# Optimization experiments

Measured on AMD Instinct MI355X. Metric: run time of the kernel, lower is better.

## Reference

```python
import jax, jax.numpy as jnp
import numpy as np
from jax import lax

V, D, L, H, MAXLEN = 32000, 512, 6, 8, 1024
DH = D // H
DFF = 4 * D
B, T = 8, 1024


def _ln(x, g, b, eps=1e-5):
    m = jnp.mean(x, axis=-1, keepdims=True)
    v = jnp.var(x, axis=-1, keepdims=True)
    return (x - m) * lax.rsqrt(v + eps) * g + b


def setup_inputs() -> dict:
    key = jax.random.key(0)
    ks = jax.random.split(key, 16)
    s = 0.02
    inp = {
        "idx": jax.random.randint(ks[0], (B, T), 0, V, dtype=jnp.int32),
        "wte": jax.random.normal(ks[1], (V, D), jnp.float32) * s,   # tied with head
        "wpe": jax.random.normal(ks[2], (MAXLEN, D), jnp.float32) * s,
        # per-layer stacked params [L, ...]
        "ln1_g": jnp.ones((L, D), jnp.float32),
        "ln1_b": jnp.zeros((L, D), jnp.float32),
        "w_qkv": jax.random.normal(ks[3], (L, D, 3 * D), jnp.float32) * s,
        "b_qkv": jnp.zeros((L, 3 * D), jnp.float32),
        "w_ao": jax.random.normal(ks[4], (L, D, D), jnp.float32) * s,
        "b_ao": jnp.zeros((L, D), jnp.float32),
        "ln2_g": jnp.ones((L, D), jnp.float32),
        "ln2_b": jnp.zeros((L, D), jnp.float32),
        "w_fc": jax.random.normal(ks[5], (L, D, DFF), jnp.float32) * s,
        "b_fc": jnp.zeros((L, DFF), jnp.float32),
        "w_pr": jax.random.normal(ks[6], (L, DFF, D), jnp.float32) * s,
        "b_pr": jnp.zeros((L, D), jnp.float32),
        "lnf_g": jnp.ones((D,), jnp.float32),
        "lnf_b": jnp.zeros((D,), jnp.float32),
    }
    return inp


def reference(idx, wte, wpe, ln1_g, ln1_b, w_qkv, b_qkv, w_ao, b_ao,
              ln2_g, ln2_b, w_fc, b_fc, w_pr, b_pr, lnf_g, lnf_b):
    Bx, Tx = idx.shape
    x = wte[idx] + wpe[:Tx]                      # [B,T,D]
    causal = jnp.tril(jnp.ones((Tx, Tx), bool))  # [T,T]
    scale = 1.0 / np.sqrt(DH)

    def block(x, p):
        (g1, b1, wqkv, bqkv, wao, bao, g2, b2, wfc, bfc, wpr, bpr) = p
        h = _ln(x, g1, b1)
        qkv = h @ wqkv + bqkv                    # [B,T,3D]
        q, k, v = jnp.split(qkv, 3, axis=-1)
        q = q.reshape(Bx, Tx, H, DH)
        k = k.reshape(Bx, Tx, H, DH)
        v = v.reshape(Bx, Tx, H, DH)
        att = jnp.einsum('bqhd,bkhd->bhqk', q, k) * scale
        att = jnp.where(causal, att, -jnp.inf)
        att = jax.nn.softmax(att, axis=-1)
        y = jnp.einsum('bhqk,bkhd->bqhd', att, v).reshape(Bx, Tx, D)
        x = x + y @ wao + bao
        h = _ln(x, g2, b2)
        h = jax.nn.gelu(h @ wfc + bfc, approximate=False)
        x = x + h @ wpr + bpr
        return x, None

    params = (ln1_g, ln1_b, w_qkv, b_qkv, w_ao, b_ao,
              ln2_g, ln2_b, w_fc, b_fc, w_pr, b_pr)
    x, _ = lax.scan(block, x, params)
    x = _ln(x, lnf_g, lnf_b)
    logits = x @ wte.T                           # tied head, [B,T,V]
    return logits
```

## Files before the change

### kernel.cpp

```cpp
#include <hip/hip_runtime.h>
#include <hip/hip_bf16.h>
#include <math.h>

#define V_   32000
#define D_   512
#define L_   6
#define H_   8
#define DH_  64
#define DFF_ 2048
#define B_   8
#define T_   1024
#define BT_  (B_*T_)

typedef __attribute__((ext_vector_type(4))) float f32x4;
typedef __attribute__((ext_vector_type(8))) short short8;
using bf16_t = __hip_bfloat16;

__device__ __forceinline__ float b2f(unsigned short u) {
    union { unsigned int i; float f; } v; v.i = ((unsigned int)u) << 16; return v.f;
}
__device__ __forceinline__ unsigned short f2b(float f) {
    bf16_t h = __float2bfloat16(f);
    return *reinterpret_cast<unsigned short*>(&h);
}
__device__ __forceinline__ void gl16(const void* g, void* l) {
    __builtin_amdgcn_global_load_lds((const __attribute__((address_space(1))) void*)g,
                                     (__attribute__((address_space(3))) void*)l, 16, 0, 0);
}
__device__ __forceinline__ float gelu_exact(float v) {
    return 0.5f * v * (1.0f + erff(v * 0.70710678118654752f));
}

__global__ __launch_bounds__(128) void embed_ln_kernel(
        const int* __restrict__ idx, const float* __restrict__ wte,
        const float* __restrict__ wpe, const float* __restrict__ g,
        const float* __restrict__ bb, float* __restrict__ x,
        bf16_t* __restrict__ hout) {
    int bt = blockIdx.x;
    int tt = bt & (T_ - 1);
    int tok = idx[bt];
    int i = threadIdx.x;
    float4 a = ((const float4*)(wte + (size_t)tok * D_))[i];
    float4 p = ((const float4*)(wpe + (size_t)tt * D_))[i];
    float4 v = make_float4(a.x + p.x, a.y + p.y, a.z + p.z, a.w + p.w);
    ((float4*)(x + (size_t)bt * D_))[i] = v;

    float s  = v.x + v.y + v.z + v.w;
    float sq = v.x*v.x + v.y*v.y + v.z*v.z + v.w*v.w;
    #pragma unroll
    for (int o = 32; o > 0; o >>= 1) {
        s  += __shfl_down(s,  o);
        sq += __shfl_down(sq, o);
    }
    __shared__ float ss[2], ssq[2];
    if ((i & 63) == 0) { ss[i >> 6] = s; ssq[i >> 6] = sq; }
    __syncthreads();
    float mean = (ss[0] + ss[1]) * (1.0f / D_);
    float var  = (ssq[0] + ssq[1]) * (1.0f / D_) - mean * mean;
    float rstd = rsqrtf(var + 1e-5f);
    float4 gg = ((const float4*)g)[i];
    float4 b2 = ((const float4*)bb)[i];
    ushort4 o4;
    o4.x = f2b((v.x - mean) * rstd * gg.x + b2.x);
    o4.y = f2b((v.y - mean) * rstd * gg.y + b2.y);
    o4.z = f2b((v.z - mean) * rstd * gg.z + b2.z);
    o4.w = f2b((v.w - mean) * rstd * gg.w + b2.w);
    ((ushort4*)(hout + (size_t)bt * D_))[i] = o4;
}

__global__ __launch_bounds__(256) void conv_kernel(
        const float* __restrict__ s, bf16_t* __restrict__ d, int n4) {
    int i = blockIdx.x * 256 + threadIdx.x;
    if (i >= n4) return;
    float4 f = ((const float4*)s)[i];
    ushort4 u = make_ushort4(f2b(f.x), f2b(f.y), f2b(f.z), f2b(f.w));
    ((ushort4*)d)[i] = u;
}

__global__ __launch_bounds__(256) void tconv_kernel(
        const float* __restrict__ src, bf16_t* __restrict__ dst, int K, int N) {
    size_t ls = (size_t)K * N;
    const float* s = src + blockIdx.z * ls;
    bf16_t* d = dst + blockIdx.z * ls;
    __shared__ float tile[32][33];
    int n0 = blockIdx.x * 32, k0 = blockIdx.y * 32;
    int c = threadIdx.x & 31, r8 = threadIdx.x >> 5;
    #pragma unroll
    for (int i = 0; i < 4; ++i) {
        int r = r8 + i * 8;
        tile[r][c] = s[(size_t)(k0 + r) * N + n0 + c];
    }
    __syncthreads();
    #pragma unroll
    for (int i = 0; i < 4; ++i) {
        int r = r8 + i * 8;
        d[(size_t)(n0 + r) * K + k0 + c] = __float2bfloat16(tile[c][r]);
    }
}

__global__ __launch_bounds__(256) void vtrans_kernel(
        const bf16_t* __restrict__ qkv, bf16_t* __restrict__ vt) {
    const unsigned short* q = (const unsigned short*)qkv;
    unsigned short* d = (unsigned short*)vt;
    __shared__ unsigned short tile[32][33];
    int bh = blockIdx.z;
    int b  = bh >> 3, h = bh & 7;
    int t0 = blockIdx.x * 32, d0 = blockIdx.y * 32;
    int c = threadIdx.x & 31, r8 = threadIdx.x >> 5;
    #pragma unroll
    for (int i = 0; i < 4; ++i) {
        int r = r8 + i * 8;
        tile[r][c] = q[(size_t)(b * T_ + t0 + r) * (3 * D_) + 2 * D_ + h * DH_ + d0 + c];
    }
    __syncthreads();
    #pragma unroll
    for (int i = 0; i < 4; ++i) {
        int r = r8 + i * 8;
        d[(size_t)(bh * DH_ + d0 + r) * T_ + t0 + c] = tile[c][r];
    }
}

template<int BK, int ACT, bool OBF, bool RES, bool CONVB>
__global__ __launch_bounds__(256) void mm_kernel(
        const bf16_t* __restrict__ A,
        const bf16_t* __restrict__ Bt,
        const float*  __restrict__ Bf,
        const float*  __restrict__ bias,
        const float*  __restrict__ res,
        void* __restrict__ Cout,
        int M, int N, int K)
{
    constexpr int SLOTS = BK / 8;
    constexpr int CH    = BK / 16;
    __shared__ __align__(16) unsigned short As[128 * BK];
    __shared__ __align__(16) unsigned short Bs[128 * BK];
    const int nwg = gridDim.x;
    const int orig = blockIdx.x;
    const int q8 = nwg >> 3, r8 = nwg & 7;
    const int xcd = orig & 7, lin = orig >> 3;
    const int wg = (xcd < r8) ? xcd * (q8 + 1) + lin
                              : r8 * (q8 + 1) + (xcd - r8) * q8 + lin;
    const int gym = M >> 7;
    const int by = wg % gym;
    const int bx = wg / gym;

    const int t    = threadIdx.x;
    const int row0 = by * 128;
    const int col0 = bx * 128;
    const int lane = t & 63;
    const int wid  = t >> 6;
    const int wm   = (wid & 1) * 64;
    const int wn   = (wid >> 1) * 64;
    const int fr   = lane & 15;
    const int fq   = lane >> 4;

    f32x4 acc[4][4];
    #pragma unroll
    for (int m = 0; m < 4; ++m)
        #pragma unroll
        for (int n = 0; n < 4; ++n)
            acc[m][n] = (f32x4)(0.0f);

    const unsigned short* Ab  = (const unsigned short*)A;
    const unsigned short* Btb = (const unsigned short*)Bt;

    for (int k0 = 0; k0 < K; k0 += BK) {
        __syncthreads();
        #pragma unroll
        for (int i = 0; i < CH; ++i) {
            int c = t + i * 256;
            int row = c / SLOTS;
            int sl  = (c & (SLOTS - 1)) ^ (row & 7);
            gl16(Ab + (size_t)(row0 + row) * K + k0 + sl * 8, As + (size_t)c * 8);
        }
        if (!CONVB) {
            #pragma unroll
            for (int i = 0; i < CH; ++i) {
                int c = t + i * 256;
                int row = c / SLOTS;
                int sl  = (c & (SLOTS - 1)) ^ (row & 7);
                gl16(Btb + (size_t)(col0 + row) * K + k0 + sl * 8, Bs + (size_t)c * 8);
            }
        } else {
            #pragma unroll
            for (int i = 0; i < CH; ++i) {
                int c = t + i * 256;
                int row = c / SLOTS;
                int sl  = (c & (SLOTS - 1)) ^ (row & 7);
                const float* sp = Bf + (size_t)(col0 + row) * K + k0 + sl * 8;
                float4 f0 = ((const float4*)sp)[0];
                float4 f1 = ((const float4*)sp)[1];
                short8 pk;
                pk[0] = f2b(f0.x); pk[1] = f2b(f0.y); pk[2] = f2b(f0.z); pk[3] = f2b(f0.w);
                pk[4] = f2b(f1.x); pk[5] = f2b(f1.y); pk[6] = f2b(f1.z); pk[7] = f2b(f1.w);
                *(short8*)(Bs + (size_t)c * 8) = pk;
            }
        }
        __syncthreads();

        #pragma unroll
        for (int kk = 0; kk < BK / 32; ++kk) {
            short8 av[4], bv[4];
            #pragma unroll
            for (int m = 0; m < 4; ++m) {
                int R = wm + m * 16 + fr;
                int sl = (kk * 4 + fq) ^ (fr & 7);
                av[m] = *(const short8*)(As + (size_t)R * BK + sl * 8);
            }
            #pragma unroll
            for (int n = 0; n < 4; ++n) {
                int R = wn + n * 16 + fr;
                int sl = (kk * 4 + fq) ^ (fr & 7);
                bv[n] = *(const short8*)(Bs + (size_t)R * BK + sl * 8);
            }
            #pragma unroll
            for (int m = 0; m < 4; ++m)
                #pragma unroll
                for (int n = 0; n < 4; ++n)
                    acc[m][n] = __builtin_amdgcn_mfma_f32_16x16x32_bf16(av[m], bv[n], acc[m][n], 0, 0, 0);
        }
    }

    #pragma unroll
    for (int n = 0; n < 4; ++n) {
        int col = col0 + wn + n * 16 + fr;
        float bb = bias ? bias[col] : 0.0f;
        #pragma unroll
        for (int m = 0; m < 4; ++m) {
            int rbase = row0 + wm + m * 16 + fq * 4;
            #pragma unroll
            for (int r = 0; r < 4; ++r) {
                float v = acc[m][n][r] + bb;
                if (ACT == 1) v = gelu_exact(v);
                size_t off = (size_t)(rbase + r) * N + col;
                if (RES) v += res[off];
                if (OBF) ((bf16_t*)Cout)[off] = __float2bfloat16(v);
                else     ((float*)Cout)[off]  = v;
            }
        }
    }
}

__global__ __launch_bounds__(512) void mm_ln_kernel(
        const bf16_t* __restrict__ A,
        const bf16_t* __restrict__ Bt,
        const float*  __restrict__ bias,
        float*        __restrict__ xio,
        const float*  __restrict__ g,
        const float*  __restrict__ lb,
        bf16_t*       __restrict__ hout,
        int M, int K)
{
    __shared__ __align__(16) unsigned short As[32 * 64];
    __shared__ __align__(16) unsigned short Bs[512 * 64];
    __shared__ float stats[32][8][2];

    const int row0 = blockIdx.x * 32;
    const int t    = threadIdx.x;
    const int lane = t & 63;
    const int w    = t >> 6;
    const int fr   = lane & 15;
    const int fq   = lane >> 4;

    const unsigned short* Ab  = (const unsigned short*)A;
    const unsigned short* Btb = (const unsigned short*)Bt;

    f32x4 acc[2][4];
    #pragma unroll
    for (int m = 0; m < 2; ++m)
        #pragma unroll
        for (int n = 0; n < 4; ++n)
            acc[m][n] = (f32x4)(0.0f);

    for (int k0 = 0; k0 < K; k0 += 64) {
        __syncthreads();
        if (t < 256) {
            int c = t;
            int row = c >> 3, sl = (c & 7) ^ (row & 7);
            gl16(Ab + (size_t)(row0 + row) * K + k0 + sl * 8, As + (size_t)c * 8);
        }
        #pragma unroll
        for (int i = 0; i < 8; ++i) {
            int c = t + i * 512;
            int row = c >> 3, sl = (c & 7) ^ (row & 7);
            gl16(Btb + (size_t)row * K + k0 + sl * 8, Bs + (size_t)c * 8);
        }
        __syncthreads();

        #pragma unroll
        for (int kk = 0; kk < 2; ++kk) {
            int sl = (kk * 4 + fq) ^ (fr & 7);
            short8 av[2], bv[4];
            #pragma unroll
            for (int m = 0; m < 2; ++m)
                av[m] = *(const short8*)(As + (size_t)(m * 16 + fr) * 64 + sl * 8);
            #pragma unroll
            for (int n = 0; n < 4; ++n)
                bv[n] = *(const short8*)(Bs + (size_t)(w * 64 + n * 16 + fr) * 64 + sl * 8);
            #pragma unroll
            for (int m = 0; m < 2; ++m)
                #pragma unroll
                for (int n = 0; n < 4; ++n)
                    acc[m][n] = __builtin_amdgcn_mfma_f32_16x16x32_bf16(av[m], bv[n], acc[m][n], 0, 0, 0);
        }
    }

    float vv[2][4][4];
    #pragma unroll
    for (int m = 0; m < 2; ++m) {
        #pragma unroll
        for (int r = 0; r < 4; ++r) {
            int rowl = m * 16 + fq * 4 + r;
            float ps = 0.0f, pq = 0.0f;
            #pragma unroll
            for (int n = 0; n < 4; ++n) {
                int col = w * 64 + n * 16 + fr;
                float v = acc[m][n][r] + bias[col] +
                          xio[(size_t)(row0 + rowl) * D_ + col];
                vv[m][n][r] = v;
                ps += v; pq += v * v;
            }
            ps += __shfl_xor(ps, 1); pq += __shfl_xor(pq, 1);
            ps += __shfl_xor(ps, 2); pq += __shfl_xor(pq, 2);
            ps += __shfl_xor(ps, 4); pq += __shfl_xor(pq, 4);
            ps += __shfl_xor(ps, 8); pq += __shfl_xor(pq, 8);
            if (fr == 0) { stats[rowl][w][0] = ps; stats[rowl][w][1] = pq; }
        }
    }
    __syncthreads();

    #pragma unroll
    for (int m = 0; m < 2; ++m) {
        #pragma unroll
        for (int r = 0; r < 4; ++r) {
            int rowl = m * 16 + fq * 4 + r;
            float su = 0.0f, sq = 0.0f;
            #pragma unroll
            for (int ww = 0; ww < 8; ++ww) {
                su += stats[rowl][ww][0];
                sq += stats[rowl][ww][1];
            }
            float mean = su * (1.0f / D_);
            float var  = sq * (1.0f / D_) - mean * mean;
            float rstd = rsqrtf(var + 1e-5f);
            #pragma unroll
            for (int n = 0; n < 4; ++n) {
                int col = w * 64 + n * 16 + fr;
                float v = vv[m][n][r];
                size_t off = (size_t)(row0 + rowl) * D_ + col;
                xio[off] = v;
                hout[off] = __float2bfloat16((v - mean) * rstd * g[col] + lb[col]);
            }
        }
    }
}

#define MM8_PHASE(MH, NH, HALF, SRCB, R0, DSTB)                               \
  {                                                                           \
    short8 af[2][4]; short8 bg[2][2];                                         \
    _Pragma("unroll")                                                         \
    for (int ks = 0; ks < 2; ++ks) {                                          \
      _Pragma("unroll")                                                       \
      for (int m = 0; m < 4; ++m) {                                           \
        int row = ((MH)*4 + m)*32 + wm*16 + fr;                               \
        int sl  = (ks*4 + fq) ^ (fr & 7);                                     \
        af[ks][m] = *(const short8*)(curA + (size_t)row*64 + (size_t)sl*8);   \
      }                                                                       \
      _Pragma("unroll")                                                       \
      for (int n = 0; n < 2; ++n) {                                           \
        int col = ((NH)*2 + n)*64 + wn*16 + fr;                               \
        int sl  = (ks*4 + fq) ^ (fr & 7);                                     \
        bg[ks][n] = *(const short8*)(curB + (size_t)col*64 + (size_t)sl*8);   \
      }                                                                       \
    }                                                                         \
    if (pf) {                                                                 \
      _Pragma("unroll")                                                       \
      for (int i = 0; i < 2; ++i) {                                           \
        int c = (HALF)*1024 + i*512 + t;                                      \
        int row = c >> 3, sl = (c & 7) ^ (row & 7);                           \
        gl16(SRCB + (size_t)((R0) + row)*K + k0n + sl*8,                      \
             DSTB + (size_t)c*8);                                             \
      }                                                                       \
      asm volatile("s_waitcnt vmcnt(2)" ::: "memory");                        \
    } else if ((MH) == 0 && (NH) == 0) {                                      \
      asm volatile("s_waitcnt vmcnt(0)" ::: "memory");                        \
    }                                                                         \
    asm volatile("s_barrier" ::: "memory");                                   \
    asm volatile("s_waitcnt lgkmcnt(0)" ::: "memory");                        \
    __builtin_amdgcn_sched_barrier(0);                                        \
    __builtin_amdgcn_s_setprio(1);                                            \
    _Pragma("unroll")                                                         \
    for (int ks = 0; ks < 2; ++ks)                                            \
      _Pragma("unroll")                                                       \
      for (int m = 0; m < 4; ++m)                                             \
        _Pragma("unroll")                                                     \
        for (int n = 0; n < 2; ++n)                                           \
          acc[(MH)*4+m][(NH)*2+n] = __builtin_amdgcn_mfma_f32_16x16x32_bf16(  \
              af[ks][m], bg[ks][n], acc[(MH)*4+m][(NH)*2+n], 0, 0, 0);        \
    __builtin_amdgcn_s_setprio(0);                                            \
    __builtin_amdgcn_sched_barrier(0);                                        \
    asm volatile("s_barrier" ::: "memory");                                   \
  }

template<int ACT, bool OBF>
__global__ __launch_bounds__(512) void mm8_kernel(
        const bf16_t* __restrict__ A,
        const bf16_t* __restrict__ Bt,
        const float*  __restrict__ bias,
        void* __restrict__ Cout,
        int M, int N, int K)
{
    __shared__ __align__(16) unsigned short sA[2][256 * 64];
    __shared__ __align__(16) unsigned short sB[2][256 * 64];

    const int nwg = gridDim.x;
    const int orig = blockIdx.x;
    const int q8 = nwg >> 3, r8 = nwg & 7;
    const int xcd = orig & 7, lin = orig >> 3;
    const int wg = (xcd < r8) ? xcd * (q8 + 1) + lin
                              : r8 * (q8 + 1) + (xcd - r8) * q8 + lin;
    const int gym = M >> 8;
    const int by = wg % gym;
    const int bx = wg / gym;
    const int row0 = by * 256;
    const int col0 = bx * 256;

    const int t    = threadIdx.x;
    const int lane = t & 63;
    const int wid  = t >> 6;
    const int wm   = wid >> 2;
    const int wn   = wid & 3;
    const int fr   = lane & 15;
    const int fq   = lane >> 4;

    const unsigned short* Ab = (const unsigned short*)A;
    const unsigned short* Bb = (const unsigned short*)Bt;

    f32x4 acc[8][4];
    #pragma unroll
    for (int m = 0; m < 8; ++m)
        #pragma unroll
        for (int n = 0; n < 4; ++n)
            acc[m][n] = (f32x4)(0.0f);

    const int NK = K >> 6;

    #pragma unroll
    for (int h = 0; h < 2; ++h)
        #pragma unroll
        for (int i = 0; i < 2; ++i) {
            int c = h * 1024 + i * 512 + t;
            int row = c >> 3, sl = (c & 7) ^ (row & 7);
            gl16(Ab + (size_t)(row0 + row) * K + sl * 8, &sA[0][(size_t)c * 8]);
            gl16(Bb + (size_t)(col0 + row) * K + sl * 8, &sB[0][(size_t)c * 8]);
        }
    asm volatile("s_waitcnt vmcnt(0)" ::: "memory");
    asm volatile("s_barrier" ::: "memory");

    for (int s = 0; s < NK; ++s) {
        const unsigned short* curA = sA[s & 1];
        const unsigned short* curB = sB[s & 1];
        unsigned short* nxA = (unsigned short*)sA[(s + 1) & 1];
        unsigned short* nxB = (unsigned short*)sB[(s + 1) & 1];
        const int k0n = (s + 1) << 6;
        const bool pf = (s + 1) < NK;
        MM8_PHASE(0, 0, 0, Ab, row0, nxA)
        MM8_PHASE(1, 0, 0, Bb, col0, nxB)
        MM8_PHASE(0, 1, 1, Ab, row0, nxA)
        MM8_PHASE(1, 1, 1, Bb, col0, nxB)
    }

    #pragma unroll
    for (int n = 0; n < 4; ++n) {
        int col = col0 + n * 64 + wn * 16 + fr;
        float bb = bias ? bias[col] : 0.0f;
        #pragma unroll
        for (int m = 0; m < 8; ++m) {
            int rbase = row0 + m * 32 + wm * 16 + fq * 4;
            #pragma unroll
            for (int r = 0; r < 4; ++r) {
                float v = acc[m][n][r] + bb;
                if (ACT == 1) v = gelu_exact(v);
                size_t off = (size_t)(rbase + r) * N + col;
                if (OBF) ((bf16_t*)Cout)[off] = __float2bfloat16(v);
                else     ((float*)Cout)[off]  = v;
            }
        }
    }
}

__global__ __launch_bounds__(512, 6) void flash_kernel(
        const bf16_t* __restrict__ qkv, const bf16_t* __restrict__ vt,
        bf16_t* __restrict__ y)
{
    __shared__ __align__(16) unsigned short Ks[2][64 * 64];
    __shared__ __align__(16) unsigned short Vs[2][64 * 64];
    __shared__ __align__(16) unsigned short Pls[128][72];

    const int qt = (T_ / 128 - 1) - (blockIdx.x >> 6);
    const int bh = blockIdx.x & 63;
    const int h  = bh & (H_ - 1);
    const int b  = bh >> 3;
    const int t  = threadIdx.x;
    const int lane = t & 63;
    const int w    = t >> 6;
    const int fr   = lane & 15;
    const int fq   = lane >> 4;
    const int srow = t >> 3;
    const int ssl  = (t & 7) ^ (srow & 7);

    const unsigned short* qkvb = (const unsigned short*)qkv;
    const unsigned short* vtb  = (const unsigned short*)vt;

    short8 avq[2];
    {
        const unsigned short* qrow = qkvb +
            (size_t)(b * T_ + qt * 128 + w * 16 + fr) * (3 * D_) + h * DH_;
        avq[0] = *(const short8*)(qrow + fq * 8);
        avq[1] = *(const short8*)(qrow + 32 + fq * 8);
    }

    float mi[4], li[4];
    f32x4 oacc[4];
    #pragma unroll
    for (int r = 0; r < 4; ++r) { mi[r] = -INFINITY; li[r] = 0.0f; }
    #pragma unroll
    for (int d = 0; d < 4; ++d) oacc[d] = (f32x4)(0.0f);

    const int nt = 2 * qt + 2;

    gl16(qkvb + (size_t)(b * T_ + srow) * (3 * D_) + D_ + h * DH_ + ssl * 8,
         &Ks[0][(size_t)t * 8]);
    gl16(vtb + (size_t)(bh * DH_ + srow) * T_ + ssl * 8,
         &Vs[0][(size_t)t * 8]);
    __syncthreads();

    for (int jt = 0; jt < nt; ++jt) {
        const int cur = jt & 1;
        if (jt + 1 < nt) {
            gl16(qkvb + (size_t)(b * T_ + (jt + 1) * 64 + srow) * (3 * D_)
                     + D_ + h * DH_ + ssl * 8,
                 &Ks[cur ^ 1][(size_t)t * 8]);
            gl16(vtb + (size_t)(bh * DH_ + srow) * T_ + (jt + 1) * 64 + ssl * 8,
                 &Vs[cur ^ 1][(size_t)t * 8]);
        }

        f32x4 s[4];
        #pragma unroll
        for (int jb = 0; jb < 4; ++jb) s[jb] = (f32x4)(0.0f);
        #pragma unroll
        for (int ks = 0; ks < 2; ++ks) {
            int sl = (ks * 4 + fq) ^ (fr & 7);
            #pragma unroll
            for (int jb = 0; jb < 4; ++jb) {
                short8 bv = *(const short8*)(&Ks[cur][(size_t)(jb * 16 + fr) * 64 + sl * 8]);
                s[jb] = __builtin_amdgcn_mfma_f32_16x16x32_bf16(avq[ks], bv, s[jb], 0, 0, 0);
            }
        }

        float sv[4][4];
        const int qgb = qt * 128 + w * 16 + fq * 4;
        #pragma unroll
        for (int jb = 0; jb < 4; ++jb) {
            int jg = jt * 64 + jb * 16 + fr;
            #pragma unroll
            for (int r = 0; r < 4; ++r) {
                float x = s[jb][r] * 0.125f;
                sv[jb][r] = (jg > qgb + r) ? -INFINITY : x;
            }
        }

        #pragma unroll
        for (int r = 0; r < 4; ++r) {
            float tm = fmaxf(fmaxf(sv[0][r], sv[1][r]), fmaxf(sv[2][r], sv[3][r]));
            tm = fmaxf(tm, __shfl_xor(tm, 1));
            tm = fmaxf(tm, __shfl_xor(tm, 2));
            tm = fmaxf(tm, __shfl_xor(tm, 4));
            tm = fmaxf(tm, __shfl_xor(tm, 8));
            float mnew = fmaxf(mi[r], tm);
            float corr = __expf(mi[r] - mnew);
            float tsum = 0.0f;
            #pragma unroll
            for (int jb = 0; jb < 4; ++jb) {
                float p = __expf(sv[jb][r] - mnew);
                sv[jb][r] = p;
                tsum += p;
            }
            tsum += __shfl_xor(tsum, 1);
            tsum += __shfl_xor(tsum, 2);
            tsum += __shfl_xor(tsum, 4);
            tsum += __shfl_xor(tsum, 8);
            li[r] = li[r] * corr + tsum;
            mi[r] = mnew;
            #pragma unroll
            for (int db = 0; db < 4; ++db) oacc[db][r] *= corr;
        }

        #pragma unroll
        for (int jb = 0; jb < 4; ++jb)
            #pragma unroll
            for (int r = 0; r < 4; ++r)
                Pls[w * 16 + fq * 4 + r][jb * 16 + fr] = f2b(sv[jb][r]);

        #pragma unroll
        for (int ks = 0; ks < 2; ++ks) {
            short8 ap = *(const short8*)(&Pls[w * 16 + fr][ks * 32 + fq * 8]);
            int sl = (ks * 4 + fq) ^ (fr & 7);
            #pragma unroll
            for (int db = 0; db < 4; ++db) {
                short8 bv = *(const short8*)(&Vs[cur][(size_t)(db * 16 + fr) * 64 + sl * 8]);
                oacc[db] = __builtin_amdgcn_mfma_f32_16x16x32_bf16(ap, bv, oacc[db], 0, 0, 0);
            }
        }

        __syncthreads();
    }

    unsigned short* yb = (unsigned short*)y;
    #pragma unroll
    for (int r = 0; r < 4; ++r) {
        float inv = 1.0f / li[r];
        size_t row = (size_t)(b * T_ + qt * 128 + w * 16 + fq * 4 + r);
        #pragma unroll
        for (int db = 0; db < 4; ++db)
            yb[row * D_ + h * DH_ + db * 16 + fr] = f2b(oacc[db][r] * inv);
    }
}

extern "C" void kernel_launch(void* const* d_in, const int* in_sizes, int n_in,
                              void* d_out, int out_size, void* d_ws, size_t ws_size,
                              hipStream_t stream) {
    const int*   idx   = (const int*)  d_in[0];
    const float* wte   = (const float*)d_in[1];
    const float* wpe   = (const float*)d_in[2];
    const float* ln1_g = (const float*)d_in[3];
    const float* ln1_b = (const float*)d_in[4];
    const float* w_qkv = (const float*)d_in[5];
    const float* b_qkv = (const float*)d_in[6];
    const float* w_ao  = (const float*)d_in[7];
    const float* b_ao  = (const float*)d_in[8];
    const float* ln2_g = (const float*)d_in[9];
    const float* ln2_b = (const float*)d_in[10];
    const float* w_fc  = (const float*)d_in[11];
    const float* b_fc  = (const float*)d_in[12];
    const float* w_pr  = (const float*)d_in[13];
    const float* b_pr  = (const float*)d_in[14];
    const float* lnf_g = (const float*)d_in[15];
    const float* lnf_b = (const float*)d_in[16];
    float* outf = (float*)d_out;

    char* base = (char*)d_out;
    size_t off = 0;
    auto alloc = [&](size_t bytes) {
        void* p = base + off;
        off += (bytes + 255) & ~(size_t)255;
        return p;
    };
    bf16_t* wqkvT = (bf16_t*)alloc((size_t)L_ * 3 * D_ * D_ * 2);
    bf16_t* waoT  = (bf16_t*)alloc((size_t)L_ * D_ * D_ * 2);
    bf16_t* wfcT  = (bf16_t*)alloc((size_t)L_ * DFF_ * D_ * 2);
    bf16_t* wprT  = (bf16_t*)alloc((size_t)L_ * D_ * DFF_ * 2);
    bf16_t* qkvb  = (bf16_t*)alloc((size_t)BT_ * 3 * D_ * 2);
    bf16_t* vtbuf = (bf16_t*)alloc((size_t)B_ * H_ * DH_ * T_ * 2);
    bf16_t* yb    = (bf16_t*)alloc((size_t)BT_ * D_ * 2);
    bf16_t* hab   = (bf16_t*)alloc((size_t)BT_ * D_ * 2);
    bf16_t* fcb   = (bf16_t*)alloc((size_t)BT_ * DFF_ * 2);
    float*  xb    = (float*) alloc((size_t)BT_ * D_ * 4);

    bf16_t* hfin = (bf16_t*)d_ws;
    size_t hbytes = ((size_t)BT_ * D_ * 2 + 255) & ~(size_t)255;
    bool wte_ws = ws_size >= hbytes + (size_t)V_ * D_ * 2 + 256;
    bf16_t* wteb = wte_ws ? (bf16_t*)((char*)d_ws + hbytes) : nullptr;

    if (wte_ws)
        conv_kernel<<<(V_ * D_ / 4 + 255) / 256, 256, 0, stream>>>(wte, wteb, V_ * D_ / 4);
    tconv_kernel<<<dim3(3 * D_ / 32, D_ / 32, L_), 256, 0, stream>>>(w_qkv, wqkvT, D_, 3 * D_);
    tconv_kernel<<<dim3(D_ / 32, D_ / 32, L_), 256, 0, stream>>>(w_ao, waoT, D_, D_);
    tconv_kernel<<<dim3(DFF_ / 32, D_ / 32, L_), 256, 0, stream>>>(w_fc, wfcT, D_, DFF_);
    tconv_kernel<<<dim3(D_ / 32, DFF_ / 32, L_), 256, 0, stream>>>(w_pr, wprT, DFF_, D_);

    embed_ln_kernel<<<BT_, 128, 0, stream>>>(idx, wte, wpe, ln1_g, ln1_b, xb, hab);

    for (int l = 0; l < L_; ++l) {
        mm8_kernel<0, true><<<(BT_ / 256) * (3 * D_ / 256), 512, 0, stream>>>(
            hab, wqkvT + (size_t)l * 3 * D_ * D_, b_qkv + (size_t)l * 3 * D_,
            qkvb, BT_, 3 * D_, D_);
        vtrans_kernel<<<dim3(T_ / 32, DH_ / 32, B_ * H_), 256, 0, stream>>>(qkvb, vtbuf);
        flash_kernel<<<512, 512, 0, stream>>>(qkvb, vtbuf, yb);
        mm_ln_kernel<<<BT_ / 32, 512, 0, stream>>>(
            yb, waoT + (size_t)l * D_ * D_, b_ao + (size_t)l * D_,
            xb, ln2_g + (size_t)l * D_, ln2_b + (size_t)l * D_, hab, BT_, D_);
        mm8_kernel<1, true><<<(BT_ / 256) * (DFF_ / 256), 512, 0, stream>>>(
            hab, wfcT + (size_t)l * DFF_ * D_, b_fc + (size_t)l * DFF_,
            fcb, BT_, DFF_, D_);
        if (l < L_ - 1)
            mm_ln_kernel<<<BT_ / 32, 512, 0, stream>>>(
                fcb, wprT + (size_t)l * D_ * DFF_, b_pr + (size_t)l * D_,
                xb, ln1_g + (size_t)(l + 1) * D_, ln1_b + (size_t)(l + 1) * D_,
                hab, BT_, DFF_);
        else
            mm_ln_kernel<<<BT_ / 32, 512, 0, stream>>>(
                fcb, wprT + (size_t)l * D_ * DFF_, b_pr + (size_t)l * D_,
                xb, lnf_g, lnf_b, hfin, BT_, DFF_);
    }

    if (wte_ws)
        mm8_kernel<0, false><<<(BT_ / 256) * (V_ / 256), 512, 0, stream>>>(
            hfin, wteb, nullptr, outf, BT_, V_, D_);
    else
        mm_kernel<64, 0, false, false, true><<<250 * 64, 256, 0, stream>>>(
            hfin, nullptr, wte, nullptr, nullptr, outf, BT_, V_, D_);
}
```

Before: 1.686 ms.

## Double-buffer B tiles in mm_ln kernel, load A directly to registers

The matmul+layernorm kernel now double-buffers the weight tile in shared memory, prefetching the next K-slice while computing the current one. A fragments are read straight from global memory into registers instead of being staged through LDS. Explicit vmcnt waits and raw barriers replace the paired __syncthreads. Float outputs of the generic matmuls are written with nontemporal stores, and flash_kernel's occupancy hint is lowered from 6 to 2. Doubling the B buffer to 128 KB of LDS caps occupancy, and the hand-written waitcnt depends on the exact load count.

```diff
diff --git a/kernel.cpp b/kernel.cpp
--- a/kernel.cpp
+++ b/kernel.cpp
@@ -235,7 +235,7 @@
                 size_t off = (size_t)(rbase + r) * N + col;
                 if (RES) v += res[off];
                 if (OBF) ((bf16_t*)Cout)[off] = __float2bfloat16(v);
-                else     ((float*)Cout)[off]  = v;
+                else     __builtin_nontemporal_store(v, (float*)Cout + off);
             }
         }
     }
@@ -251,8 +251,7 @@
         bf16_t*       __restrict__ hout,
         int M, int K)
 {
-    __shared__ __align__(16) unsigned short As[32 * 64];
-    __shared__ __align__(16) unsigned short Bs[512 * 64];
+    __shared__ __align__(16) unsigned short Bs[2][512 * 64];
     __shared__ float stats[32][8][2];
 
     const int row0 = blockIdx.x * 32;
@@ -272,37 +271,53 @@
         for (int n = 0; n < 4; ++n)
             acc[m][n] = (f32x4)(0.0f);
 
-    for (int k0 = 0; k0 < K; k0 += 64) {
-        __syncthreads();
-        if (t < 256) {
-            int c = t;
-            int row = c >> 3, sl = (c & 7) ^ (row & 7);
-            gl16(Ab + (size_t)(row0 + row) * K + k0 + sl * 8, As + (size_t)c * 8);
-        }
-        #pragma unroll
-        for (int i = 0; i < 8; ++i) {
-            int c = t + i * 512;
-            int row = c >> 3, sl = (c & 7) ^ (row & 7);
-            gl16(Btb + (size_t)row * K + k0 + sl * 8, Bs + (size_t)c * 8);
-        }
-        __syncthreads();
-
+    const int NS = K >> 6;
+
+    #pragma unroll
+    for (int i = 0; i < 8; ++i) {
+        int c = t + i * 512;
+        int row = c >> 3, sl = (c & 7) ^ (row & 7);
+        gl16(Btb + (size_t)row * K + sl * 8, &Bs[0][(size_t)c * 8]);
+    }
+
+    for (int s = 0; s < NS; ++s) {
+        const int k0 = s << 6;
+        short8 av[2][2];
+        #pragma unroll
+        for (int ks = 0; ks < 2; ++ks)
+            #pragma unroll
+            for (int m = 0; m < 2; ++m)
+                av[ks][m] = *(const short8*)(
+                    Ab + (size_t)(row0 + m * 16 + fr) * K + k0 + (ks * 4 + fq) * 8);
+        if (s + 1 < NS) {
+            #pragma unroll
+            for (int i = 0; i < 8; ++i) {
+                int c = t + i * 512;
+                int row = c >> 3, sl = (c & 7) ^ (row & 7);
+                gl16(Btb + (size_t)row * K + (k0 + 64) + sl * 8,
+                     &Bs[(s + 1) & 1][(size_t)c * 8]);
+            }
+            asm volatile("s_waitcnt vmcnt(8)" ::: "memory");
+        } else {
+            asm volatile("s_waitcnt vmcnt(0)" ::: "memory");
+        }
+        asm volatile("s_barrier" ::: "memory");
+
+        const unsigned short* cb = Bs[s & 1];
         #pragma unroll
         for (int kk = 0; kk < 2; ++kk) {
             int sl = (kk * 4 + fq) ^ (fr & 7);
-            short8 av[2], bv[4];
-            #pragma unroll
-            for (int m = 0; m < 2; ++m)
-                av[m] = *(const short8*)(As + (size_t)(m * 16 + fr) * 64 + sl * 8);
+            short8 bv[4];
             #pragma unroll
             for (int n = 0; n < 4; ++n)
-                bv[n] = *(const short8*)(Bs + (size_t)(w * 64 + n * 16 + fr) * 64 + sl * 8);
+                bv[n] = *(const short8*)(cb + (size_t)(w * 64 + n * 16 + fr) * 64 + sl * 8);
             #pragma unroll
             for (int m = 0; m < 2; ++m)
                 #pragma unroll
                 for (int n = 0; n < 4; ++n)
-                    acc[m][n] = __builtin_amdgcn_mfma_f32_16x16x32_bf16(av[m], bv[n], acc[m][n], 0, 0, 0);
-        }
+                    acc[m][n] = __builtin_amdgcn_mfma_f32_16x16x32_bf16(av[kk][m], bv[n], acc[m][n], 0, 0, 0);
+        }
+        asm volatile("s_barrier" ::: "memory");
     }
 
     float vv[2][4][4];
@@ -483,13 +498,13 @@
                 if (ACT == 1) v = gelu_exact(v);
                 size_t off = (size_t)(rbase + r) * N + col;
                 if (OBF) ((bf16_t*)Cout)[off] = __float2bfloat16(v);
-                else     ((float*)Cout)[off]  = v;
-            }
-        }
-    }
-}
-
-__global__ __launch_bounds__(512, 6) void flash_kernel(
+                else     __builtin_nontemporal_store(v, (float*)Cout + off);
+            }
+        }
+    }
+}
+
+__global__ __launch_bounds__(512, 2) void flash_kernel(
         const bf16_t* __restrict__ qkv, const bf16_t* __restrict__ vt,
         bf16_t* __restrict__ y)
 {
```

After: 1.870 ms. 10.9% more time.
